# Optimization experiments

Hardware: AMD Instinct MI355X
Metric: run time of the kernel (lower is better)

Reference implementation:

```python
import jax, jax.numpy as jnp
import numpy as np
import math

B, T, D = 2, 2048, 1024
H, DH = 16, 64  # n_heads, d_head
ROPE_THETA = 10000.0


def _rope_cos_sin(seq_len, d_head, dtype):
    # inv_freq over even indices, freqs[i,j] = t_i * inv_freq_j, shape [T, d_head//2]
    inv_freq = 1.0 / (ROPE_THETA ** (jnp.arange(0, d_head, 2, dtype=jnp.float32) / d_head))
    freqs = jnp.arange(seq_len, dtype=jnp.float32)[:, None] * inv_freq[None, :]
    # emb = cat(freqs, freqs); we only ever index cos[..., :d_head//2], so keep the half
    cos = jnp.cos(freqs).astype(dtype)[None, :, None, :]  # [1,T,1,DH/2]
    sin = jnp.sin(freqs).astype(dtype)[None, :, None, :]
    return cos, sin


def _apply_rotation(x, cos, sin):
    # x: [B,T,H,DH]; rotate-half style as in the torch module
    x1, x2 = x[..., : x.shape[-1] // 2], x[..., x.shape[-1] // 2 :]
    return jnp.concatenate([x1 * cos - x2 * sin, x1 * sin + x2 * cos], axis=-1)


def setup_inputs() -> dict:
    key = jax.random.key(0)
    k1, k2, k3 = jax.random.split(key, 3)
    x = jax.random.normal(k1, (B, T, D), dtype=jnp.float32)
    # torch Linear weights stored transposed here as [in, out]; init_std=0.02
    Wqkv = jax.random.normal(k2, (D, 3 * D), dtype=jnp.float32) * 0.02
    Wout = jax.random.normal(k3, (D, D), dtype=jnp.float32) * 0.02
    return {"x": x, "Wqkv": Wqkv, "Wout": Wout}


def reference(x, Wqkv, Wout):
    b, t, d = x.shape
    qkv = x @ Wqkv  # [B,T,3D]
    q, k, v = jnp.split(qkv, 3, axis=-1)
    q = q.reshape(b, t, H, DH)
    k = k.reshape(b, t, H, DH)
    v = v.reshape(b, t, H, DH)

    cos, sin = _rope_cos_sin(t, DH, x.dtype)
    q = _apply_rotation(q, cos, sin)
    k = _apply_rotation(k, cos, sin)

    scale = 1.0 / math.sqrt(DH)
    # scores: [B,H,Tq,Tk]
    scores = jnp.einsum("bqhd,bkhd->bhqk", q, k) * scale
    causal = jnp.triu(jnp.ones((t, t), dtype=bool), k=1)
    scores = jnp.where(causal[None, None, :, :], -jnp.inf, scores)
    attn = jax.nn.softmax(scores, axis=-1)
    # dropout in eval mode -> identity
    out = jnp.einsum("bhqk,bkhd->bqhd", attn, v).reshape(b, t, d)
    return out @ Wout
```

## Files before the change

kernel.cpp:

```cpp
#include <hip/hip_runtime.h>
#include <hip/hip_bf16.h>
#include <stdint.h>
#include <math.h>

#define T_SEQ 2048
#define NHEAD 16
#define NBH   32
#define BTROW 4096

typedef __bf16 bf16_t;
typedef __bf16 bf16x4_t __attribute__((ext_vector_type(4)));
typedef __bf16 bf16x8_t __attribute__((ext_vector_type(8)));
typedef float  f32x4_t  __attribute__((ext_vector_type(4)));

#define QSCALE 0.18033688011112042f

__device__ __forceinline__ f32x4_t mfma16(bf16x8_t a, bf16x8_t b, f32x4_t c) {
  return __builtin_amdgcn_mfma_f32_16x16x32_bf16(a, b, c, 0, 0, 0);
}

__device__ __forceinline__ float fast_exp2(float x) {
#if __has_builtin(__builtin_amdgcn_exp2f)
  return __builtin_amdgcn_exp2f(x);
#else
  return exp2f(x);
#endif
}

__device__ __forceinline__ void gl_lds16(const bf16_t* g, bf16_t* l) {
  __builtin_amdgcn_global_load_lds(
      (const __attribute__((address_space(1))) void*)g,
      (__attribute__((address_space(3))) void*)l, 16, 0, 0);
}

__device__ __forceinline__ int tile_off(int r, int k8) {
  int lr = r >> 1;
  int g = (((r & 1) << 2) | k8) ^ (lr & 7);
  return lr * 64 + g * 8;
}
__device__ __forceinline__ int src_off(int c, int K) {
  int lr = c >> 3;
  int gsrc = (c & 7) ^ (lr & 7);
  int row = (lr << 1) | (gsrc >> 2), kb = gsrc & 3;
  return row * K + kb * 8;
}

__device__ __forceinline__ void trans_tile(const float* __restrict__ W,
                                           bf16_t* __restrict__ WT,
                                           int K, int N, int n0, int k0,
                                           float (*tile)[33], int tid) {
  int tx = tid & 31, ty = tid >> 5;
#pragma unroll
  for (int j = 0; j < 4; j++)
    tile[ty + j * 8][tx] = W[(size_t)(k0 + ty + j * 8) * N + n0 + tx];
  __syncthreads();
#pragma unroll
  for (int j = 0; j < 4; j++)
    WT[(size_t)(n0 + ty + j * 8) * K + k0 + tx] = (bf16_t)tile[tx][ty + j * 8];
}

__global__ __launch_bounds__(256) void k_prep(const float* __restrict__ x,
                                              const float* __restrict__ Wqkv,
                                              const float* __restrict__ Wout,
                                              bf16_t* __restrict__ xb,
                                              bf16_t* __restrict__ wqkvT,
                                              bf16_t* __restrict__ woutT,
                                              float* __restrict__ cs,
                                              float* __restrict__ sn) {
  __shared__ float tile[32][33];
  int blk = blockIdx.x, tid = threadIdx.x;
  if (blk < 2048) {
    const int n = 4096 * 1024, stride = 2048 * 256;
    for (int i = (blk * 256 + tid) * 4; i < n; i += stride * 4) {
      float4 a = *(const float4*)(x + i);
      bf16x4_t r = { (bf16_t)a.x, (bf16_t)a.y, (bf16_t)a.z, (bf16_t)a.w };
      *(bf16x4_t*)(xb + i) = r;
    }
  } else if (blk < 5120) {
    int bb = blk - 2048;
    trans_tile(Wqkv, wqkvT, 1024, 3072, (bb % 96) * 32, (bb / 96) * 32, tile, tid);
  } else if (blk < 6144) {
    int bb = blk - 5120;
    trans_tile(Wout, woutT, 1024, 1024, (bb % 32) * 32, (bb / 32) * 32, tile, tid);
  } else {
    int i = (blk - 6144) * 256 + tid;
    int t = i >> 5, j = i & 31;
    float inv = powf(10000.0f, -(float)(2 * j) / 64.0f);
    float f = (float)t * inv;
    cs[i] = cosf(f);
    sn[i] = sinf(f);
  }
}

__global__ __launch_bounds__(256) void k_gemm_qkv(const bf16_t* __restrict__ A,
                                                  const bf16_t* __restrict__ Bt,
                                                  const float* __restrict__ cs,
                                                  const float* __restrict__ sn,
                                                  bf16_t* __restrict__ Qr,
                                                  bf16_t* __restrict__ Kr,
                                                  bf16_t* __restrict__ Vt) {
  const int K = 1024, NT = 32;
  __shared__ __align__(16) unsigned char smem[49152];
  bf16_t* vtile = (bf16_t*)smem;

  int m0 = blockIdx.y * 128, n0 = blockIdx.x * 128;
  int tid = threadIdx.x;
  int lane = tid & 63, w = tid >> 6;
  int wr = w >> 1, wc = w & 1;
  int l15 = lane & 15, l4 = lane >> 4;

  f32x4_t acc[4][4];
#pragma unroll
  for (int m = 0; m < 4; m++)
#pragma unroll
    for (int n = 0; n < 4; n++) acc[m][n] = (f32x4_t){0.f, 0.f, 0.f, 0.f};

  const bf16_t* Ag = A + (size_t)m0 * K;
  const bf16_t* Bg = Bt + (size_t)n0 * K;
  int soff0 = src_off(tid, K), soff1 = src_off(256 + tid, K);
  int dst0 = w * 512, dst1 = 2048 + w * 512;
  int afo[4], bfo[4];
#pragma unroll
  for (int m = 0; m < 4; m++) afo[m] = tile_off(wr * 64 + m * 16 + l15, l4);
#pragma unroll
  for (int n = 0; n < 4; n++) bfo[n] = tile_off(wc * 64 + n * 16 + l15, l4);

  auto stageg = [&](int bufbyte, int k0) {
    bf16_t* As = (bf16_t*)(smem + bufbyte);
    bf16_t* Bs = (bf16_t*)(smem + 8192 + bufbyte);
    gl_lds16(Ag + soff0 + k0, As + dst0);
    gl_lds16(Bg + soff0 + k0, Bs + dst0);
    gl_lds16(Ag + soff1 + k0, As + dst1);
    gl_lds16(Bg + soff1 + k0, Bs + dst1);
  };

#define QKV_BODY(KT, CB)                                                          \
  {                                                                               \
    if ((KT) + 1 < NT) asm volatile("s_waitcnt vmcnt(4)" ::: "memory");           \
    else               asm volatile("s_waitcnt vmcnt(0)" ::: "memory");           \
    __builtin_amdgcn_s_barrier();                                                 \
    if ((KT) + 2 < NT) stageg((((CB) + 2) % 3) * 16384, ((KT) + 2) * 32);         \
    const bf16_t* As = (const bf16_t*)(smem + (CB) * 16384);                      \
    const bf16_t* Bs = (const bf16_t*)(smem + 8192 + (CB) * 16384);               \
    bf16x8_t af[4], bfr[4];                                                       \
    _Pragma("unroll")                                                             \
    for (int m = 0; m < 4; m++) af[m] = *(const bf16x8_t*)(As + afo[m]);          \
    _Pragma("unroll")                                                             \
    for (int n = 0; n < 4; n++) bfr[n] = *(const bf16x8_t*)(Bs + bfo[n]);         \
    _Pragma("unroll")                                                             \
    for (int m = 0; m < 4; m++)                                                   \
      _Pragma("unroll")                                                           \
      for (int n = 0; n < 4; n++) acc[m][n] = mfma16(af[m], bfr[n], acc[m][n]);   \
  }

  stageg(0, 0);
  stageg(16384, 32);
  for (int kt0 = 0; kt0 < 30; kt0 += 3) {
    QKV_BODY(kt0 + 0, 0)
    QKV_BODY(kt0 + 1, 1)
    QKV_BODY(kt0 + 2, 2)
  }
  QKV_BODY(30, 0)
  QKV_BODY(31, 1)
#undef QKV_BODY
  __syncthreads();

  int region = n0 >> 10;
  if (region < 2) {
    bf16_t* dst = region ? Kr : Qr;
    float qs = region ? 1.0f : QSCALE;
    int h = ((n0 & 1023) + wc * 64) >> 6;
#pragma unroll
    for (int m = 0; m < 4; m++)
#pragma unroll
      for (int r = 0; r < 4; r++) {
        int row = m0 + wr * 64 + m * 16 + l4 * 4 + r;
        int b = row >> 11, t = row & 2047;
        size_t obase = ((size_t)(b * NHEAD + h) * T_SEQ + t) * 64;
#pragma unroll
        for (int n = 0; n < 2; n++) {
          int j = n * 16 + l15;
          float c = cs[t * 32 + j], s = sn[t * 32 + j];
          float x1 = acc[m][n][r], x2 = acc[m][n + 2][r];
          dst[obase + j]      = (bf16_t)((x1 * c - x2 * s) * qs);
          dst[obase + 32 + j] = (bf16_t)((x1 * s + x2 * c) * qs);
        }
      }
  } else {
#pragma unroll
    for (int m = 0; m < 4; m++)
#pragma unroll
      for (int n = 0; n < 4; n++)
#pragma unroll
        for (int r = 0; r < 4; r++)
          vtile[(size_t)(wc * 64 + n * 16 + l15) * 132 + wr * 64 + m * 16 + l4 * 4 + r] =
              (bf16_t)acc[m][n][r];
    __syncthreads();
    int colbase = n0 - 2048;
    int b = m0 >> 11, t0l = m0 & 2047;
#pragma unroll
    for (int p = 0; p < 64; p++) {
      int idx = p * 256 + tid;
      int dl = idx >> 7, tl = idx & 127;
      int col = colbase + dl, h = col >> 6, d = col & 63;
      Vt[((size_t)(b * NHEAD + h) * 64 + d) * T_SEQ + t0l + tl] = vtile[(size_t)dl * 132 + tl];
    }
  }
}

__global__ __launch_bounds__(256) void k_gemm2(const bf16_t* __restrict__ A,
                                               const bf16_t* __restrict__ Bt,
                                               float* __restrict__ C) {
  const int N = 1024, K = 1024, NT = 32;
  __shared__ __align__(16) unsigned char smem[36864];
  int m0 = blockIdx.y * 64, n0 = blockIdx.x * 128;
  int tid = threadIdx.x;
  int lane = tid & 63, w = tid >> 6;
  int l15 = lane & 15, l4 = lane >> 4;

  f32x4_t acc[4][2];
#pragma unroll
  for (int m = 0; m < 4; m++)
#pragma unroll
    for (int n = 0; n < 2; n++) acc[m][n] = (f32x4_t){0.f, 0.f, 0.f, 0.f};

  const bf16_t* Ag = A + (size_t)m0 * K;
  const bf16_t* Bg = Bt + (size_t)n0 * K;
  int soff0 = src_off(tid, K), soff1 = src_off(256 + tid, K);
  int dstA = w * 512, dstB0 = w * 512, dstB1 = 2048 + w * 512;
  int afo[4], bfo[2];
#pragma unroll
  for (int m = 0; m < 4; m++) afo[m] = tile_off(m * 16 + l15, l4);
#pragma unroll
  for (int n = 0; n < 2; n++) bfo[n] = tile_off(w * 32 + n * 16 + l15, l4);

  auto stageg = [&](int bufbyte, int k0) {
    bf16_t* As = (bf16_t*)(smem + bufbyte);
    bf16_t* Bs = (bf16_t*)(smem + 4096 + bufbyte);
    gl_lds16(Ag + soff0 + k0, As + dstA);
    gl_lds16(Bg + soff0 + k0, Bs + dstB0);
    gl_lds16(Bg + soff1 + k0, Bs + dstB1);
  };

#define G2_BODY(KT, CB)                                                           \
  {                                                                               \
    if ((KT) + 1 < NT) asm volatile("s_waitcnt vmcnt(3)" ::: "memory");           \
    else               asm volatile("s_waitcnt vmcnt(0)" ::: "memory");           \
    __builtin_amdgcn_s_barrier();                                                 \
    if ((KT) + 2 < NT) stageg((((CB) + 2) % 3) * 12288, ((KT) + 2) * 32);         \
    const bf16_t* As = (const bf16_t*)(smem + (CB) * 12288);                      \
    const bf16_t* Bs = (const bf16_t*)(smem + 4096 + (CB) * 12288);               \
    bf16x8_t af[4], bfr[2];                                                       \
    _Pragma("unroll")                                                             \
    for (int m = 0; m < 4; m++) af[m] = *(const bf16x8_t*)(As + afo[m]);          \
    _Pragma("unroll")                                                             \
    for (int n = 0; n < 2; n++) bfr[n] = *(const bf16x8_t*)(Bs + bfo[n]);         \
    _Pragma("unroll")                                                             \
    for (int m = 0; m < 4; m++)                                                   \
      _Pragma("unroll")                                                           \
      for (int n = 0; n < 2; n++) acc[m][n] = mfma16(af[m], bfr[n], acc[m][n]);   \
  }

  stageg(0, 0);
  stageg(12288, 32);
  for (int kt0 = 0; kt0 < 30; kt0 += 3) {
    G2_BODY(kt0 + 0, 0)
    G2_BODY(kt0 + 1, 1)
    G2_BODY(kt0 + 2, 2)
  }
  G2_BODY(30, 0)
  G2_BODY(31, 1)
#undef G2_BODY

#pragma unroll
  for (int m = 0; m < 4; m++)
#pragma unroll
    for (int n = 0; n < 2; n++)
#pragma unroll
      for (int r = 0; r < 4; r++) {
        int row = m0 + m * 16 + l4 * 4 + r;
        int col = n0 + w * 32 + n * 16 + l15;
        C[(size_t)row * N + col] = acc[m][n][r];
      }
}

__global__ __launch_bounds__(512, 4) void k_attn(const bf16_t* __restrict__ Qr,
                                                 const bf16_t* __restrict__ Kr,
                                                 const bf16_t* __restrict__ Vt,
                                                 bf16_t* __restrict__ Ob) {
  __shared__ __align__(16) bf16_t Ks[2][64 * 64];
  __shared__ __align__(16) bf16_t Vs[2][2][64 * 64];
  __shared__ __align__(16) bf16_t Ps[8][16 * 64];
  int flat = blockIdx.x;
  int swz = (flat & 7) * 64 + (flat >> 3);
  int pair = swz & 15, bh = swz >> 4;
  int b = bh >> 4, h = bh & 15;
  int tid = threadIdx.x, lane = tid & 63, w = tid >> 6;
  int grp = w >> 2, wl = w & 3;
  int l15 = lane & 15, l4 = lane >> 4;

  const bf16_t* Kbh = Kr + (size_t)bh * T_SEQ * 64;
  const bf16_t* Vbh = Vt + (size_t)bh * 64 * T_SEQ;

  int srow = tid >> 3;
  int sk8 = (tid & 7) ^ (srow & 7);

  auto stageK = [&](int i) {
#pragma unroll
    for (int tp = 0; tp < 2; tp++) {
      int kb = (2 * i + tp) * 64;
      gl_lds16(Kbh + (size_t)(kb + srow) * 64 + sk8 * 8, &Ks[tp][0] + (size_t)w * 512);
    }
  };
  auto stageV = [&](int buf, int i) {
#pragma unroll
    for (int tp = 0; tp < 2; tp++) {
      int kb = (2 * i + tp) * 64;
      gl_lds16(Vbh + (size_t)srow * T_SEQ + kb + sk8 * 8, &Vs[buf][tp][0] + (size_t)w * 512);
    }
  };

  char* myPs = (char*)&Ps[w][0];

  bf16x8_t ones;
#pragma unroll
  for (int i = 0; i < 8; i++) ones[i] = (bf16_t)1.0f;

  for (int pass = 0; pass < 2; pass++) {
    int qb = pass ? (31 - pair) : pair;
    int q0 = qb * 64;
    int niter = (qb + 2) >> 1;

    bf16x8_t qf[2];
    size_t qbase = ((size_t)bh * T_SEQ + q0 + wl * 16 + l15) * 64;
    qf[0] = *(const bf16x8_t*)(Qr + qbase + l4 * 8);
    qf[1] = *(const bf16x8_t*)(Qr + qbase + 32 + l4 * 8);

    f32x4_t o[4];
#pragma unroll
    for (int n = 0; n < 4; n++) o[n] = (f32x4_t){0.f, 0.f, 0.f, 0.f};
    f32x4_t ls = (f32x4_t){0.f, 0.f, 0.f, 0.f};
    float m_s = -1e30f;

    stageK(0);
    stageV(0, 0);
    asm volatile("s_waitcnt vmcnt(0)" ::: "memory");
    __builtin_amdgcn_s_barrier();

    for (int i = 0; i < niter; i++) {
      int cur = i & 1;
      int t = 2 * i + grp;
      bool act = (t <= qb);

      f32x4_t s[4];
      if (act) {
        const bf16_t* Kt = &Ks[grp][0];
        __builtin_amdgcn_s_setprio(1);
#pragma unroll
        for (int n = 0; n < 4; n++) {
          int rowK = n * 16 + l15;
          const bf16_t* kp = Kt + (size_t)rowK * 64;
          int sw = rowK & 7;
          bf16x8_t kf0 = *(const bf16x8_t*)(kp + (l4 ^ sw) * 8);
          bf16x8_t kf1 = *(const bf16x8_t*)(kp + ((l4 ^ 4) ^ sw) * 8);
          s[n] = (f32x4_t){0.f, 0.f, 0.f, 0.f};
          s[n] = mfma16(kf0, qf[0], s[n]);
          s[n] = mfma16(kf1, qf[1], s[n]);
        }
        __builtin_amdgcn_s_setprio(0);
      }
      __builtin_amdgcn_s_barrier();

      if (i + 1 < niter) {
        stageK(i + 1);
        stageV(cur ^ 1, i + 1);
      }

      if (act) {
        const bf16_t* Vtl = &Vs[cur][grp][0];
        bf16x8_t vfr[8];
#pragma unroll
        for (int ks = 0; ks < 2; ks++)
#pragma unroll
          for (int n = 0; n < 4; n++) {
            int rowV = n * 16 + l15;
            vfr[ks * 4 + n] = *(const bf16x8_t*)(Vtl + (size_t)rowV * 64 +
                                                 (((ks * 4 + l4) ^ (rowV & 7)) * 8));
          }

        if (t == qb) {
#pragma unroll
          for (int n = 0; n < 4; n++)
#pragma unroll
            for (int r = 0; r < 4; r++)
              if (n * 16 + l4 * 4 + r > wl * 16 + l15) s[n][r] = -1e30f;
        }

        float t0 = fmaxf(fmaxf(s[0][0], s[0][1]), fmaxf(s[0][2], s[0][3]));
        float t1 = fmaxf(fmaxf(s[1][0], s[1][1]), fmaxf(s[1][2], s[1][3]));
        float t2 = fmaxf(fmaxf(s[2][0], s[2][1]), fmaxf(s[2][2], s[2][3]));
        float t3 = fmaxf(fmaxf(s[3][0], s[3][1]), fmaxf(s[3][2], s[3][3]));
        float mloc = fmaxf(fmaxf(t0, t1), fmaxf(t2, t3));

        if (__any(mloc - m_s > 8.0f)) {
          float mx = fmaxf(mloc, __shfl_xor(mloc, 16, 64));
          mx = fmaxf(mx, __shfl_xor(mx, 32, 64));
          float mnew = fmaxf(m_s, mx);
          float alpha = fast_exp2(m_s - mnew);
          m_s = mnew;
          float ar[4];
#pragma unroll
          for (int r = 0; r < 4; r++) ar[r] = __shfl(alpha, l4 * 4 + r, 64);
#pragma unroll
          for (int n = 0; n < 4; n++)
#pragma unroll
            for (int r = 0; r < 4; r++) o[n][r] *= ar[r];
#pragma unroll
          for (int r = 0; r < 4; r++) ls[r] *= ar[r];
        }

#pragma unroll
        for (int n = 0; n < 4; n++) {
#pragma unroll
          for (int r = 0; r < 4; r++) s[n][r] = fast_exp2(s[n][r] - m_s);
          bf16x4_t pk = { (bf16_t)s[n][0], (bf16_t)s[n][1], (bf16_t)s[n][2], (bf16_t)s[n][3] };
          *(bf16x4_t*)(myPs + l15 * 128 +
                       ((((n << 1) | (l4 >> 1)) ^ (l15 & 7)) << 4) + ((l4 & 1) << 3)) = pk;
        }

        __builtin_amdgcn_s_setprio(1);
#pragma unroll
        for (int ks = 0; ks < 2; ks++) {
          bf16x8_t pa = *(const bf16x8_t*)(myPs + l15 * 128 +
                                           ((((ks << 2) | l4) ^ (l15 & 7)) << 4));
          ls = mfma16(pa, ones, ls);
#pragma unroll
          for (int n = 0; n < 4; n++) o[n] = mfma16(pa, vfr[ks * 4 + n], o[n]);
        }
        __builtin_amdgcn_s_setprio(0);
      }

      asm volatile("s_waitcnt vmcnt(0)" ::: "memory");
      __builtin_amdgcn_s_barrier();
    }

    __syncthreads();
    float* mg = (float*)&Vs[0][0][0];
    int base = (wl * 64 + lane) * 25;
    if (grp == 1) {
#pragma unroll
      for (int n = 0; n < 4; n++)
#pragma unroll
        for (int r = 0; r < 4; r++) mg[base + n * 4 + r] = o[n][r];
#pragma unroll
      for (int r = 0; r < 4; r++) mg[base + 16 + r] = ls[r];
#pragma unroll
      for (int r = 0; r < 4; r++) mg[base + 20 + r] = __shfl(m_s, l4 * 4 + r, 64);
    }
    __syncthreads();
    if (grp == 0) {
#pragma unroll
      for (int r = 0; r < 4; r++) {
        float mA = __shfl(m_s, l4 * 4 + r, 64);
        float mB = mg[base + 20 + r];
        float mF = fmaxf(mA, mB);
        float fA = fast_exp2(mA - mF), fB = fast_exp2(mB - mF);
        float lF = ls[r] * fA + mg[base + 16 + r] * fB;
        float ir = 1.0f / lF;
        int q = q0 + wl * 16 + l4 * 4 + r;
        size_t off = ((size_t)(b * T_SEQ + q)) * 1024 + h * 64;
#pragma unroll
        for (int n = 0; n < 4; n++) {
          float val = o[n][r] * fA + mg[base + n * 4 + r] * fB;
          Ob[off + n * 16 + l15] = (bf16_t)(val * ir);
        }
      }
    }
    __syncthreads();
  }
}

extern "C" void kernel_launch(void* const* d_in, const int* in_sizes, int n_in,
                              void* d_out, int out_size, void* d_ws, size_t ws_size,
                              hipStream_t stream) {
  const float* x    = (const float*)d_in[0];
  const float* Wqkv = (const float*)d_in[1];
  const float* Wout = (const float*)d_in[2];
  float* out = (float*)d_out;
  char* ws = (char*)d_ws;

  bf16_t* wqkvT = (bf16_t*)(ws + 0);
  bf16_t* woutT = (bf16_t*)(ws + 6291456);
  bf16_t* xb    = (bf16_t*)(ws + 8388608);
  bf16_t* Qr    = (bf16_t*)(ws + 41943040);
  bf16_t* Kr    = (bf16_t*)(ws + 50331648);
  bf16_t* Vt    = (bf16_t*)(ws + 58720256);
  float*  cs    = (float*)(ws + 67108864);
  float*  sn    = (float*)(ws + 67371008);
  bf16_t* Ob    = xb;

  k_prep<<<6400, 256, 0, stream>>>(x, Wqkv, Wout, xb, wqkvT, woutT, cs, sn);
  k_gemm_qkv<<<dim3(3072 / 128, 4096 / 128), 256, 0, stream>>>(xb, wqkvT, cs, sn, Qr, Kr, Vt);
  k_attn<<<512, 512, 0, stream>>>(Qr, Kr, Vt, Ob);
  k_gemm2<<<dim3(1024 / 128, 4096 / 64), 256, 0, stream>>>(Ob, woutT, out);
}
```

Measured before the change: 99.25 us.

## Load V fragments directly from global in attention; swizzle gemm2 block order

The attention kernel stops staging V tiles through shared memory and instead has each wave load its V fragments straight from global memory into registers at the start of each iteration. This shrinks LDS use from the double-buffered V arrays down to 32KB, which may allow more resident blocks, and removes LDS write/read traffic for V. The trade-off is uncoalesced, latency-exposed global loads on the critical path. Separately, the output GEMM switches to a 1D grid with a swizzled block-to-tile mapping to improve cache locality.

```diff
diff --git a/kernel.cpp b/kernel.cpp
--- a/kernel.cpp
+++ b/kernel.cpp
@@ -213,7 +213,9 @@
                                                float* __restrict__ C) {
   const int N = 1024, K = 1024, NT = 32;
   __shared__ __align__(16) unsigned char smem[36864];
-  int m0 = blockIdx.y * 64, n0 = blockIdx.x * 128;
+  int flat = blockIdx.x;
+  int swz = (flat & 7) * 64 + (flat >> 3);
+  int m0 = (swz >> 3) * 64, n0 = (swz & 7) * 128;
   int tid = threadIdx.x;
   int lane = tid & 63, w = tid >> 6;
   int l15 = lane & 15, l4 = lane >> 4;
@@ -288,9 +290,9 @@
                                                  const bf16_t* __restrict__ Kr,
                                                  const bf16_t* __restrict__ Vt,
                                                  bf16_t* __restrict__ Ob) {
-  __shared__ __align__(16) bf16_t Ks[2][64 * 64];
-  __shared__ __align__(16) bf16_t Vs[2][2][64 * 64];
-  __shared__ __align__(16) bf16_t Ps[8][16 * 64];
+  __shared__ __align__(16) unsigned char sm[32768];
+  bf16_t* Ks = (bf16_t*)sm;
+  char* PsB = (char*)(sm + 16384);
   int flat = blockIdx.x;
   int swz = (flat & 7) * 64 + (flat >> 3);
   int pair = swz & 15, bh = swz >> 4;
@@ -309,18 +311,18 @@
 #pragma unroll
     for (int tp = 0; tp < 2; tp++) {
       int kb = (2 * i + tp) * 64;
-      gl_lds16(Kbh + (size_t)(kb + srow) * 64 + sk8 * 8, &Ks[tp][0] + (size_t)w * 512);
+      gl_lds16(Kbh + (size_t)(kb + srow) * 64 + sk8 * 8, Ks + tp * 4096 + (size_t)w * 512);
     }
   };
-  auto stageV = [&](int buf, int i) {
-#pragma unroll
-    for (int tp = 0; tp < 2; tp++) {
-      int kb = (2 * i + tp) * 64;
-      gl_lds16(Vbh + (size_t)srow * T_SEQ + kb + sk8 * 8, &Vs[buf][tp][0] + (size_t)w * 512);
-    }
-  };
-
-  char* myPs = (char*)&Ps[w][0];
+
+  char* myPs = PsB + w * 2048;
+
+  const bf16_t* vbase[8];
+#pragma unroll
+  for (int ks = 0; ks < 2; ks++)
+#pragma unroll
+    for (int n = 0; n < 4; n++)
+      vbase[ks * 4 + n] = Vbh + (size_t)(n * 16 + l15) * T_SEQ + ks * 32 + l4 * 8;
 
   bf16x8_t ones;
 #pragma unroll
@@ -343,18 +345,21 @@
     float m_s = -1e30f;
 
     stageK(0);
-    stageV(0, 0);
     asm volatile("s_waitcnt vmcnt(0)" ::: "memory");
     __builtin_amdgcn_s_barrier();
 
     for (int i = 0; i < niter; i++) {
-      int cur = i & 1;
       int t = 2 * i + grp;
       bool act = (t <= qb);
+      int kb = t * 64;
 
       f32x4_t s[4];
+      bf16x8_t vfr[8];
       if (act) {
-        const bf16_t* Kt = &Ks[grp][0];
+#pragma unroll
+        for (int j = 0; j < 8; j++) vfr[j] = *(const bf16x8_t*)(vbase[j] + kb);
+
+        const bf16_t* Kt = Ks + grp * 4096;
         __builtin_amdgcn_s_setprio(1);
 #pragma unroll
         for (int n = 0; n < 4; n++) {
@@ -371,23 +376,9 @@
       }
       __builtin_amdgcn_s_barrier();
 
-      if (i + 1 < niter) {
-        stageK(i + 1);
-        stageV(cur ^ 1, i + 1);
-      }
+      if (i + 1 < niter) stageK(i + 1);
 
       if (act) {
-        const bf16_t* Vtl = &Vs[cur][grp][0];
-        bf16x8_t vfr[8];
-#pragma unroll
-        for (int ks = 0; ks < 2; ks++)
-#pragma unroll
-          for (int n = 0; n < 4; n++) {
-            int rowV = n * 16 + l15;
-            vfr[ks * 4 + n] = *(const bf16x8_t*)(Vtl + (size_t)rowV * 64 +
-                                                 (((ks * 4 + l4) ^ (rowV & 7)) * 8));
-          }
-
         if (t == qb) {
 #pragma unroll
           for (int n = 0; n < 4; n++)
@@ -445,7 +436,7 @@
     }
 
     __syncthreads();
-    float* mg = (float*)&Vs[0][0][0];
+    float* mg = (float*)sm;
     int base = (wl * 64 + lane) * 25;
     if (grp == 1) {
 #pragma unroll
@@ -502,5 +493,5 @@
   k_prep<<<6400, 256, 0, stream>>>(x, Wqkv, Wout, xb, wqkvT, woutT, cs, sn);
   k_gemm_qkv<<<dim3(3072 / 128, 4096 / 128), 256, 0, stream>>>(xb, wqkvT, cs, sn, Qr, Kr, Vt);
   k_attn<<<512, 512, 0, stream>>>(Qr, Kr, Vt, Ob);
-  k_gemm2<<<dim3(1024 / 128, 4096 / 64), 256, 0, stream>>>(Ob, woutT, out);
-}
+  k_gemm2<<<512, 256, 0, stream>>>(Ob, woutT, out);
+}
```

Measured after the change: 138.7 us. 1.4x slower.
